# Kernel tuning notes

Hardware: AMD Instinct MI355X
Metric: run time of the kernel (lower is better)

## Reference

```python
import jax, jax.numpy as jnp
import numpy as np

D = 768
NH = 12
HD = D // NH
T = 8
HW = 14
B = 16
BT = B * T
NTOK = 1 + HW * HW  # 197
DH = int(D * 0.25)  # adapter hidden = 192
SCALE = 0.5


def _ln(x, g, b, eps=1e-5):
    # fp32 LayerNorm (matches LayerNorm subclass casting to fp32)
    xf = x.astype(jnp.float32)
    m = xf.mean(-1, keepdims=True)
    v = ((xf - m) ** 2).mean(-1, keepdims=True)
    return (((xf - m) / jnp.sqrt(v + eps)) * g + b).astype(x.dtype)


def _adapter(x, w1, b1, w2, b2, skip):
    h = jax.nn.gelu(x @ w1.T + b1, approximate=False)
    h = h @ w2.T + b2
    return x + h if skip else h


def _attention(xq, ykv, in_w, in_b, out_w, out_b):
    # xq: [Tx, N, D], ykv: [Ty, N, D]
    q = xq @ in_w[:D].T + in_b[:D]
    k = ykv @ in_w[D:2 * D].T + in_b[D:2 * D]
    v = ykv @ in_w[2 * D:].T + in_b[2 * D:]
    Tx, N, _ = q.shape
    Ty = k.shape[0]
    q = q.reshape(Tx, N, NH, HD).transpose(1, 2, 0, 3)  # [N,h,Tx,hd]
    k = k.reshape(Ty, N, NH, HD).transpose(1, 2, 0, 3)
    v = v.reshape(Ty, N, NH, HD).transpose(1, 2, 0, 3)
    aff = jnp.einsum('nhqd,nhkd->nhqk', q, k) / jnp.asarray(np.sqrt(HD), q.dtype)
    aff = jax.nn.softmax(aff, axis=-1)
    out = jnp.einsum('nhqk,nhkd->nhqd', aff, v)
    out = out.transpose(2, 0, 1, 3).reshape(Tx, N, D)
    return out @ out_w.T + out_b


_SHIFTS = (((0, 0), -4), ((0, 1), 1), ((1, 0), -1), ((0, 2), 2),
           ((2, 0), -2), ((1, 2), 3), ((2, 1), -3), ((2, 2), 4))


def _patch_shift(x):
    # x: [B, T, H, W, C]; roll along time on strided spatial grids
    out = x
    for (i, j), s in _SHIFTS:
        out = out.at[:, :, i::3, j::3, :].set(jnp.roll(x[:, :, i::3, j::3, :], s, axis=1))
    return out


def _forward(x, in_w, in_b, out_w, out_b, ln1_g, ln1_b, ln2_g, ln2_b,
             fc_w, fc_b, proj_w, proj_b,
             t1_w, t1_b, t2_w, t2_b,
             s1_w, s1_b, s2_w, s2_b,
             m1_w, m1_b, m2_w, m2_b):
    n, bt, d = x.shape
    b = bt // T
    # temporal attention on class token
    cls = x[:1]  # [1, bt, d]
    xt = cls.reshape(1, b, T, d).transpose(2, 1, 0, 3).reshape(T, b, d)
    xtn = _ln(xt, ln1_g, ln1_b)
    xt = _attention(xtn, xtn, in_w, in_b, out_w, out_b)
    xt = _adapter(xt, t1_w, t1_b, t2_w, t2_b, skip=False)
    xt = xt.reshape(T, b, 1, d).transpose(2, 1, 0, 3).reshape(1, bt, d)
    x = jnp.concatenate([x[:1], xt, x[1:]], axis=0)  # [n+1, bt, d]
    # spatial attention with patch shift (extra shifted K/V tokens)
    xln = _ln(x, ln1_g, ln1_b)
    tmp = xln[2:]  # [HW*HW, bt, d]
    tmp = tmp.reshape(HW, HW, b, T, d).transpose(2, 3, 0, 1, 4)  # b t h w c
    tmp = _patch_shift(tmp)
    tmp = tmp.transpose(2, 3, 0, 1, 4).reshape(HW * HW, bt, d)
    kv = jnp.concatenate([xln, tmp], axis=0)  # [2n+... , bt, d]
    attn_out = _attention(xln, kv, in_w, in_b, out_w, out_b)
    x = x + _adapter(attn_out, s1_w, s1_b, s2_w, s2_b, skip=True)
    # drop temporal token
    x = jnp.concatenate([x[:1], x[2:]], axis=0)
    # MLP + scaled MLP adapter
    xn = _ln(x, ln2_g, ln2_b)
    h = xn @ fc_w.T + fc_b
    h = h * jax.nn.sigmoid(1.702 * h)  # QuickGELU
    mlp = h @ proj_w.T + proj_b
    x = x + mlp + SCALE * _adapter(xn, m1_w, m1_b, m2_w, m2_b, skip=False)
    return x


def setup_inputs() -> dict:
    key = jax.random.key(0)
    ks = jax.random.split(key, 16)
    s = 0.02
    inp = {
        'x': jax.random.normal(ks[0], (NTOK, BT, D), jnp.float32),
        'in_w': jax.random.normal(ks[1], (3 * D, D), jnp.float32) * s,
        'in_b': jnp.zeros((3 * D,), jnp.float32),
        'out_w': jax.random.normal(ks[2], (D, D), jnp.float32) * s,
        'out_b': jnp.zeros((D,), jnp.float32),
        'ln1_g': jnp.ones((D,), jnp.float32),
        'ln1_b': jnp.zeros((D,), jnp.float32),
        'ln2_g': jnp.ones((D,), jnp.float32),
        'ln2_b': jnp.zeros((D,), jnp.float32),
        'fc_w': jax.random.normal(ks[3], (4 * D, D), jnp.float32) * s,
        'fc_b': jnp.zeros((4 * D,), jnp.float32),
        'proj_w': jax.random.normal(ks[4], (D, 4 * D), jnp.float32) * s,
        'proj_b': jnp.zeros((D,), jnp.float32),
        't1_w': jax.random.normal(ks[5], (DH, D), jnp.float32) * s,
        't1_b': jnp.zeros((DH,), jnp.float32),
        't2_w': jax.random.normal(ks[6], (D, DH), jnp.float32) * s,
        't2_b': jnp.zeros((D,), jnp.float32),
        's1_w': jax.random.normal(ks[7], (DH, D), jnp.float32) * s,
        's1_b': jnp.zeros((DH,), jnp.float32),
        's2_w': jax.random.normal(ks[8], (D, DH), jnp.float32) * s,
        's2_b': jnp.zeros((D,), jnp.float32),
        'm1_w': jax.random.normal(ks[9], (DH, D), jnp.float32) * s,
        'm1_b': jnp.zeros((DH,), jnp.float32),
        'm2_w': jax.random.normal(ks[10], (D, DH), jnp.float32) * s,
        'm2_b': jnp.zeros((D,), jnp.float32),
    }
    return inp


def reference(x, in_w, in_b, out_w, out_b, ln1_g, ln1_b, ln2_g, ln2_b,
              fc_w, fc_b, proj_w, proj_b,
              t1_w, t1_b, t2_w, t2_b,
              s1_w, s1_b, s2_w, s2_b,
              m1_w, m1_b, m2_w, m2_b):
    return _forward(x, in_w, in_b, out_w, out_b, ln1_g, ln1_b, ln2_g, ln2_b,
                    fc_w, fc_b, proj_w, proj_b,
                    t1_w, t1_b, t2_w, t2_b,
                    s1_w, s1_b, s2_w, s2_b,
                    m1_w, m1_b, m2_w, m2_b)
```

## Files before the change

### kernel.cpp

```cpp
#include <hip/hip_runtime.h>
#include <hip/hip_bf16.h>


#define DEV static __device__ __forceinline__

constexpr int D     = 768;
constexpr int TT    = 8;
constexpr int BT    = 128;
constexpr int NTOK  = 197;
constexpr int NTOK2 = 198;
constexpr int NKV   = 394;
constexpr int NKVP  = 448;
constexpr int NQP   = 224;
constexpr int NSZ   = 64;
constexpr int MQ    = NTOK2 * NSZ;
constexpr int MKV   = NKV   * NSZ;

constexpr int R2 = NTOK2 * BT;
constexpr int R3 = NTOK  * BT;

constexpr size_t O_WB  = 0;
constexpr size_t O_XLN = 3981312;
constexpr size_t O_AO  = O_XLN + 9732096;
constexpr size_t O_QT  = O_AO  + 9732096;
constexpr size_t O_KT  = O_QT  + 5505024;
constexpr size_t O_VT  = O_KT  + 11010048;
constexpr size_t O_SM  = O_VT  + 11010048;
constexpr size_t O_XT   = O_SM;
constexpr size_t O_XTN  = O_XT  + 98304;
constexpr size_t O_QKVT = O_XTN + 49152;
constexpr size_t O_AT   = O_QKVT+ 294912;
constexpr size_t O_ATP  = O_AT  + 49152;
constexpr size_t O_TH   = O_ATP + 49152;
constexpr size_t O_XT2  = O_TH  + 12288;
constexpr size_t O_MQ   = O_XT2 + 98304;
constexpr size_t O_MKV  = O_MQ  + 12672;

constexpr size_t WB_INW = 0;
constexpr size_t WB_OUTW= 1769472;
constexpr size_t WB_FCW = 2359296;
constexpr size_t WB_PJW = 4718592;
constexpr size_t WB_T1W = 7077888;
constexpr size_t WB_T2W = 7225344;
constexpr size_t WB_S1W = 7372800;
constexpr size_t WB_S2W = 7520256;
constexpr size_t WB_M1W = 7667712;
constexpr size_t WB_M2W = 7815168;

typedef __attribute__((ext_vector_type(8))) short bf16x8;
typedef __attribute__((ext_vector_type(4))) float f32x4;
#define MFMA16 __builtin_amdgcn_mfma_f32_16x16x32_bf16

DEV float bf2f(unsigned short u) { return __uint_as_float(((unsigned)u) << 16); }
DEV unsigned short f2bf(float f) {
    unsigned u = __float_as_uint(f);
    u += 0x7fffu + ((u >> 16) & 1u);
    return (unsigned short)(u >> 16);
}

__global__ __launch_bounds__(256) void convert_k(const float* __restrict__ src,
                                                 unsigned short* __restrict__ dst, int n)
{
    int i = blockIdx.x * 256 + threadIdx.x;
    if (i < n) dst[i] = f2bf(src[i]);
}

template<int EPI, int OMODE>
__global__ __launch_bounds__(256) void gemm_mfma_k(
    const unsigned short* __restrict__ A, const int* __restrict__ rowmap,
    const unsigned short* __restrict__ Wb, int wlda,
    const float* __restrict__ bias, float bscale,
    float* __restrict__ Yf, unsigned short* __restrict__ Yb, int N, int K)
{
    __shared__ unsigned short Als[128][40];
    __shared__ unsigned short Wls[64][40];
    const int tid = threadIdx.x;
    const int n0 = blockIdx.x * 64, m0 = blockIdx.y * 128;
    const int w = tid >> 6, l = tid & 63;

    const int sr = tid >> 2, sseg = tid & 3;
    int gr1 = m0 + sr, gr2 = m0 + 64 + sr;
    if (rowmap) { gr1 = rowmap[gr1]; gr2 = rowmap[gr2]; }
    const unsigned short* Ap1 = A + (size_t)gr1 * K + sseg * 8;
    const unsigned short* Ap2 = A + (size_t)gr2 * K + sseg * 8;
    const unsigned short* Wp  = Wb + (size_t)(n0 + sr) * wlda + sseg * 8;

    f32x4 acc[2][4];
    #pragma unroll
    for (int r = 0; r < 2; ++r)
        #pragma unroll
        for (int c = 0; c < 4; ++c)
            acc[r][c] = (f32x4){0.f, 0.f, 0.f, 0.f};

    for (int k0 = 0; k0 < K; k0 += 32) {
        __syncthreads();
        *(uint4*)&Als[sr][sseg * 8]      = *(const uint4*)(Ap1 + k0);
        *(uint4*)&Als[64 + sr][sseg * 8] = *(const uint4*)(Ap2 + k0);
        *(uint4*)&Wls[sr][sseg * 8]      = *(const uint4*)(Wp  + k0);
        __syncthreads();

        bf16x8 af[2], bfr[4];
        #pragma unroll
        for (int r = 0; r < 2; ++r)
            af[r] = *(const bf16x8*)&Als[w * 32 + r * 16 + (l & 15)][(l >> 4) * 8];
        #pragma unroll
        for (int c = 0; c < 4; ++c)
            bfr[c] = *(const bf16x8*)&Wls[c * 16 + (l & 15)][(l >> 4) * 8];
        #pragma unroll
        for (int r = 0; r < 2; ++r)
            #pragma unroll
            for (int c = 0; c < 4; ++c)
                acc[r][c] = MFMA16(af[r], bfr[c], acc[r][c], 0, 0, 0);
    }

    #pragma unroll
    for (int r = 0; r < 2; ++r) {
        #pragma unroll
        for (int c = 0; c < 4; ++c) {
            const int colg = n0 + c * 16 + (l & 15);
            const float bv = bscale * bias[colg];
            #pragma unroll
            for (int i = 0; i < 4; ++i) {
                const int rowg = m0 + w * 32 + r * 16 + ((l >> 4) << 2) + i;
                float v = acc[r][c][i] + bv;
                if (EPI == 1) v = 0.5f * v * (1.f + erff(v * 0.70710678118654752f));
                else if (EPI == 2) v = v / (1.f + __expf(-1.702f * v));
                if (OMODE == 0) {
                    Yf[(size_t)rowg * N + colg] = v;
                } else if (OMODE == 1) {
                    Yb[(size_t)rowg * N + colg] = f2bf(v);
                } else if (OMODE == 3) {
                    int j = rowg >> 6, bbl = rowg & 63, h = colg >> 6, d = colg & 63;
                    Yb[(((size_t)bbl * 12 + h) * NKVP + j) * 64 + d] = f2bf(v);
                } else if (OMODE == 4) {
                    int j = rowg >> 6, bbl = rowg & 63, h = colg >> 6, d = colg & 63;
                    Yb[(((size_t)bbl * 12 + h) * 64 + d) * NKVP + j] = f2bf(v);
                } else if (OMODE == 5) {
                    int j = rowg >> 6, bbl = rowg & 63, h = colg >> 6, d = colg & 63;
                    Yb[(((size_t)bbl * 12 + h) * NQP + j) * 64 + d] = f2bf(v * 0.125f);
                } else if (OMODE == 6) {
                    Yf[(size_t)rowg * N + colg] += v;
                } else if (OMODE == 7) {
                    Yf[(size_t)rowg * N + colg] += 0.5f * v;
                }
            }
        }
    }
}

template<typename TO>
__global__ __launch_bounds__(256) void ln_k(
    const float* __restrict__ in, TO* __restrict__ out,
    const float* __restrict__ g, const float* __restrict__ b, int rows)
{
    int w = (int)((blockIdx.x * 256 + threadIdx.x) >> 6);
    int lane = threadIdx.x & 63;
    if (w >= rows) return;
    const float* x = in + (size_t)w * D;
    float v[12];
    float s = 0.f;
    #pragma unroll
    for (int i = 0; i < 12; ++i) { v[i] = x[lane + 64 * i]; s += v[i]; }
    #pragma unroll
    for (int m = 32; m; m >>= 1) s += __shfl_xor(s, m);
    float mean = s * (1.f / 768.f);
    float s2 = 0.f;
    #pragma unroll
    for (int i = 0; i < 12; ++i) { float d0 = v[i] - mean; s2 += d0 * d0; }
    #pragma unroll
    for (int m = 32; m; m >>= 1) s2 += __shfl_xor(s2, m);
    float rstd = rsqrtf(s2 * (1.f / 768.f) + 1e-5f);
    TO* o = out + (size_t)w * D;
    #pragma unroll
    for (int i = 0; i < 12; ++i) {
        int c = lane + 64 * i;
        float y = (v[i] - mean) * rstd * g[c] + b[c];
        if constexpr (sizeof(TO) == 2) o[c] = f2bf(y); else o[c] = y;
    }
}

__global__ __launch_bounds__(256) void ln_gather_k(
    const float* __restrict__ x, const float* __restrict__ xt2,
    unsigned short* __restrict__ out,
    const float* __restrict__ g, const float* __restrict__ b)
{
    int w = (int)((blockIdx.x * 256 + threadIdx.x) >> 6);
    int lane = threadIdx.x & 63;
    if (w >= R2) return;
    int tok = w >> 7, bb = w & 127;
    const float* src;
    if (tok == 0)      src = x + (size_t)bb * D;
    else if (tok == 1) src = xt2 + (size_t)((bb & 7) * 16 + (bb >> 3)) * D;
    else               src = x + ((size_t)(tok - 1) * BT + bb) * D;
    float v[12];
    float s = 0.f;
    #pragma unroll
    for (int i = 0; i < 12; ++i) { v[i] = src[lane + 64 * i]; s += v[i]; }
    #pragma unroll
    for (int m = 32; m; m >>= 1) s += __shfl_xor(s, m);
    float mean = s * (1.f / 768.f);
    float s2 = 0.f;
    #pragma unroll
    for (int i = 0; i < 12; ++i) { float d0 = v[i] - mean; s2 += d0 * d0; }
    #pragma unroll
    for (int m = 32; m; m >>= 1) s2 += __shfl_xor(s2, m);
    float rstd = rsqrtf(s2 * (1.f / 768.f) + 1e-5f);
    unsigned short* o = out + (size_t)w * D;
    #pragma unroll
    for (int i = 0; i < 12; ++i) {
        int c = lane + 64 * i;
        o[c] = f2bf((v[i] - mean) * rstd * g[c] + b[c]);
    }
}

__global__ __launch_bounds__(256) void gather_cls_k(const float* __restrict__ x, float* __restrict__ xt)
{
    int idx = blockIdx.x * 256 + threadIdx.x;
    if (idx >= 128 * 768) return;
    int row = idx / 768, c = idx % 768;
    int t = row >> 4, bsel = row & 15;
    xt[idx] = x[(size_t)(bsel * TT + t) * D + c];
}

__global__ __launch_bounds__(64) void attn_temporal_k(
    const float* __restrict__ QKVt, unsigned short* __restrict__ Ot)
{
    int n = blockIdx.x, h = blockIdx.y;
    int lane = threadIdx.x;
    __shared__ float qs[8][64], ks[8][64], vs[8][64];
    __shared__ float ps[8][9];
    {
        int t = lane >> 3, f8 = lane & 7;
        size_t rb = ((size_t)(t * 16 + n)) * 2304 + h * 64 + f8 * 8;
        *(float4*)&qs[t][f8 * 8]     = *(const float4*)&QKVt[rb];
        *(float4*)&qs[t][f8 * 8 + 4] = *(const float4*)&QKVt[rb + 4];
        *(float4*)&ks[t][f8 * 8]     = *(const float4*)&QKVt[rb + 768];
        *(float4*)&ks[t][f8 * 8 + 4] = *(const float4*)&QKVt[rb + 772];
        *(float4*)&vs[t][f8 * 8]     = *(const float4*)&QKVt[rb + 1536];
        *(float4*)&vs[t][f8 * 8 + 4] = *(const float4*)&QKVt[rb + 1540];
    }
    __syncthreads();
    int qt = lane >> 3, kt = lane & 7;
    float s = 0.f;
    #pragma unroll
    for (int d0 = 0; d0 < 64; ++d0) s += qs[qt][d0] * ks[kt][d0];
    s *= 0.125f;
    float mx = s;
    #pragma unroll
    for (int m = 4; m; m >>= 1) mx = fmaxf(mx, __shfl_xor(mx, m));
    float p = __expf(s - mx), sum = p;
    #pragma unroll
    for (int m = 4; m; m >>= 1) sum += __shfl_xor(sum, m);
    ps[qt][kt] = p / sum;
    __syncthreads();
    int dg = lane & 7;
    float o[8] = {};
    #pragma unroll
    for (int k2 = 0; k2 < 8; ++k2) {
        float pp = ps[qt][k2];
        #pragma unroll
        for (int dd = 0; dd < 8; ++dd) o[dd] += pp * vs[k2][dg * 8 + dd];
    }
    unsigned short* op = &Ot[((size_t)(qt * 16 + n)) * D + h * 64 + dg * 8];
    #pragma unroll
    for (int dd = 0; dd < 8; ++dd) op[dd] = f2bf(o[dd]);
}

__global__ __launch_bounds__(256) void build_maps_k(int* __restrict__ mq,
                                                    int* __restrict__ mkv, int nbase)
{
    int idx = blockIdx.x * 256 + threadIdx.x;
    if (idx < MQ) {
        int j = idx >> 6, bbl = idx & 63;
        mq[idx] = j * BT + nbase + bbl;
    }
    int k = idx - MQ;
    if (k >= 0 && k < MKV) {
        int j = k >> 6, bb = nbase + (k & 63);
        int src;
        if (j < NTOK2) src = j * BT + bb;
        else {
            const int stab[9] = {-4, 1, 2, -1, 0, 3, -2, -3, 4};
            int p = j - NTOK2, r = p / 14, c = p % 14;
            int s = stab[(r % 3) * 3 + (c % 3)];
            int b = bb >> 3, t = bb & 7;
            int t2 = (t - s) & 7;
            src = (2 + p) * BT + b * TT + t2;
        }
        mkv[k] = src;
    }
}

__global__ __launch_bounds__(256) void attn_mfma_k(
    const unsigned short* __restrict__ Qt, const unsigned short* __restrict__ Kt,
    const unsigned short* __restrict__ Vt, unsigned short* __restrict__ AO, int nbase)
{
    const int qt0 = blockIdx.x * 32;
    const int h = blockIdx.y, nloc = blockIdx.z;
    const int tid = threadIdx.x, w = tid >> 6, l = tid & 63;
    __shared__ float Sls[32][68];
    __shared__ unsigned short Pls[32][72];
    __shared__ float mrun[32], lrun[32], alphals[32];

    const size_t baseQ = ((size_t)(nloc * 12 + h)) * NQP * 64;
    const size_t baseK = ((size_t)(nloc * 12 + h)) * NKVP * 64;
    const size_t baseV = ((size_t)(nloc * 12 + h)) * 64 * NKVP;

    bf16x8 qf[2][2];
    #pragma unroll
    for (int qb = 0; qb < 2; ++qb)
        #pragma unroll
        for (int ds = 0; ds < 2; ++ds)
            qf[qb][ds] = *(const bf16x8*)&Qt[baseQ + (size_t)(qt0 + qb * 16 + (l & 15)) * 64 + ds * 32 + (l >> 4) * 8];

    if (tid < 32) { mrun[tid] = -3e30f; lrun[tid] = 0.f; }
    f32x4 of[2];
    of[0] = (f32x4){0.f, 0.f, 0.f, 0.f};
    of[1] = (f32x4){0.f, 0.f, 0.f, 0.f};
    __syncthreads();

    for (int kv0 = 0; kv0 < NKV; kv0 += 64) {
        f32x4 sa[2];
        sa[0] = (f32x4){0.f, 0.f, 0.f, 0.f};
        sa[1] = (f32x4){0.f, 0.f, 0.f, 0.f};
        #pragma unroll
        for (int ds = 0; ds < 2; ++ds) {
            bf16x8 kf = *(const bf16x8*)&Kt[baseK + (size_t)(kv0 + w * 16 + (l & 15)) * 64 + ds * 32 + (l >> 4) * 8];
            #pragma unroll
            for (int qb = 0; qb < 2; ++qb)
                sa[qb] = MFMA16(qf[qb][ds], kf, sa[qb], 0, 0, 0);
        }
        #pragma unroll
        for (int qb = 0; qb < 2; ++qb)
            #pragma unroll
            for (int i = 0; i < 4; ++i)
                Sls[qb * 16 + ((l >> 4) << 2) + i][w * 16 + (l & 15)] = sa[qb][i];
        __syncthreads();

        {
            int row = tid >> 3, cg = tid & 7;
            float sv[8], pv[8];
            float mx = -3e30f;
            #pragma unroll
            for (int j = 0; j < 8; ++j) {
                int c = cg * 8 + j;
                float s = (kv0 + c < NKV) ? Sls[row][c] : -3e30f;
                sv[j] = s; mx = fmaxf(mx, s);
            }
            mx = fmaxf(mx, __shfl_xor(mx, 1));
            mx = fmaxf(mx, __shfl_xor(mx, 2));
            mx = fmaxf(mx, __shfl_xor(mx, 4));
            float mold = mrun[row];
            float mnew = fmaxf(mold, mx);
            float ps = 0.f;
            #pragma unroll
            for (int j = 0; j < 8; ++j) { float p = __expf(sv[j] - mnew); pv[j] = p; ps += p; }
            ps += __shfl_xor(ps, 1);
            ps += __shfl_xor(ps, 2);
            ps += __shfl_xor(ps, 4);
            if (cg == 0) {
                float al = __expf(mold - mnew);
                alphals[row] = al;
                mrun[row] = mnew;
                lrun[row] = lrun[row] * al + ps;
            }
            #pragma unroll
            for (int j = 0; j < 8; ++j) Pls[row][cg * 8 + j] = f2bf(pv[j]);
        }
        __syncthreads();

        #pragma unroll
        for (int qb = 0; qb < 2; ++qb) {
            #pragma unroll
            for (int i = 0; i < 4; ++i)
                of[qb][i] *= alphals[qb * 16 + ((l >> 4) << 2) + i];
        }
        #pragma unroll
        for (int ks = 0; ks < 2; ++ks) {
            bf16x8 vf = *(const bf16x8*)&Vt[baseV + (size_t)(w * 16 + (l & 15)) * NKVP + kv0 + ks * 32 + (l >> 4) * 8];
            #pragma unroll
            for (int qb = 0; qb < 2; ++qb) {
                bf16x8 pf = *(const bf16x8*)&Pls[qb * 16 + (l & 15)][ks * 32 + (l >> 4) * 8];
                of[qb] = MFMA16(pf, vf, of[qb], 0, 0, 0);
            }
        }
        __syncthreads();
    }

    #pragma unroll
    for (int qb = 0; qb < 2; ++qb) {
        #pragma unroll
        for (int i = 0; i < 4; ++i) {
            int qrow = qb * 16 + ((l >> 4) << 2) + i;
            int q = qt0 + qrow;
            if (q < NTOK2) {
                float inv = 1.f / lrun[qrow];
                AO[((size_t)q * BT + nbase + nloc) * D + h * 64 + w * 16 + (l & 15)] = f2bf(of[qb][i] * inv);
            }
        }
    }
}

__global__ __launch_bounds__(256) void residual_drop_k(
    const float* __restrict__ x, const unsigned short* __restrict__ ao2b,
    const unsigned short* __restrict__ sadb, float* __restrict__ out)
{
    int idx = blockIdx.x * 256 + threadIdx.x;
    int tok = idx / (BT * D), rest = idx % (BT * D);
    int stok = tok ? tok + 1 : 0;
    size_t s = (size_t)stok * BT * D + rest;
    size_t sx = (stok == 0) ? (size_t)rest : (size_t)(stok - 1) * BT * D + rest;
    out[idx] = x[sx] + bf2f(ao2b[s]) + bf2f(sadb[s]);
}

extern "C" void kernel_launch(void* const* d_in, const int* in_sizes, int n_in,
                              void* d_out, int out_size, void* d_ws, size_t ws_size,
                              hipStream_t stream)
{
    const float* x    = (const float*)d_in[0];
    const float* in_w = (const float*)d_in[1];
    const float* in_b = (const float*)d_in[2];
    const float* outw = (const float*)d_in[3];
    const float* outb = (const float*)d_in[4];
    const float* ln1g = (const float*)d_in[5];
    const float* ln1b = (const float*)d_in[6];
    const float* ln2g = (const float*)d_in[7];
    const float* ln2b = (const float*)d_in[8];
    const float* fcw  = (const float*)d_in[9];
    const float* fcb  = (const float*)d_in[10];
    const float* pjw  = (const float*)d_in[11];
    const float* pjb  = (const float*)d_in[12];
    const float* t1w  = (const float*)d_in[13];
    const float* t1b  = (const float*)d_in[14];
    const float* t2w  = (const float*)d_in[15];
    const float* t2b  = (const float*)d_in[16];
    const float* s1w  = (const float*)d_in[17];
    const float* s1b  = (const float*)d_in[18];
    const float* s2w  = (const float*)d_in[19];
    const float* s2b  = (const float*)d_in[20];
    const float* m1w  = (const float*)d_in[21];
    const float* m1b  = (const float*)d_in[22];
    const float* m2w  = (const float*)d_in[23];
    const float* m2b  = (const float*)d_in[24];

    float* ws  = (float*)d_ws;
    float* out = (float*)d_out;

    unsigned short* WB = (unsigned short*)(ws + O_WB);
    unsigned short* w_in  = WB + WB_INW;
    unsigned short* w_out = WB + WB_OUTW;
    unsigned short* w_fc  = WB + WB_FCW;
    unsigned short* w_pj  = WB + WB_PJW;
    unsigned short* w_t1  = WB + WB_T1W;
    unsigned short* w_t2  = WB + WB_T2W;
    unsigned short* w_s1  = WB + WB_S1W;
    unsigned short* w_s2  = WB + WB_S2W;
    unsigned short* w_m1  = WB + WB_M1W;
    unsigned short* w_m2  = WB + WB_M2W;

    unsigned short* xln  = (unsigned short*)(ws + O_XLN);
    unsigned short* AO   = (unsigned short*)(ws + O_AO);
    unsigned short* Qt   = (unsigned short*)(ws + O_QT);
    unsigned short* Kt   = (unsigned short*)(ws + O_KT);
    unsigned short* Vt   = (unsigned short*)(ws + O_VT);
    unsigned short* ao2b = xln;
    unsigned short* xn   = AO;
    unsigned short* h192 = Qt;
    unsigned short* h19m = Qt;
    unsigned short* sadb = Kt;
    unsigned short* hfcb = Vt;

    float* xt            = ws + O_XT;
    unsigned short* xtn  = (unsigned short*)(ws + O_XTN);
    float* qkvt          = ws + O_QKVT;
    unsigned short* at   = (unsigned short*)(ws + O_AT);
    unsigned short* atp  = (unsigned short*)(ws + O_ATP);
    unsigned short* th   = (unsigned short*)(ws + O_TH);
    float* xt2           = ws + O_XT2;
    int*   mapq          = (int*)(ws + O_MQ);
    int*   mapkv         = (int*)(ws + O_MKV);

    auto conv = [&](const float* s, unsigned short* dst, int n) {
        convert_k<<<(n + 255) / 256, 256, 0, stream>>>(s, dst, n);
    };
    conv(in_w, w_in, 2304 * 768);
    conv(outw, w_out, 768 * 768);
    conv(fcw,  w_fc,  3072 * 768);
    conv(pjw,  w_pj,  768 * 3072);
    conv(t1w,  w_t1,  192 * 768);
    conv(t2w,  w_t2,  768 * 192);
    conv(s1w,  w_s1,  192 * 768);
    conv(s2w,  w_s2,  768 * 192);
    conv(m1w,  w_m1,  192 * 768);
    conv(m2w,  w_m2,  768 * 192);

    gather_cls_k<<<384, 256, 0, stream>>>(x, xt);
    ln_k<unsigned short><<<32, 256, 0, stream>>>(xt, xtn, ln1g, ln1b, 128);
    gemm_mfma_k<0,0><<<dim3(36,1), 256, 0, stream>>>(xtn, nullptr, w_in, 768, in_b, 1.f, qkvt, nullptr, 2304, 768);
    attn_temporal_k<<<dim3(16,12), 64, 0, stream>>>(qkvt, at);
    gemm_mfma_k<0,1><<<dim3(12,1), 256, 0, stream>>>(at,  nullptr, w_out, 768, outb, 1.f, nullptr, atp, 768, 768);
    gemm_mfma_k<1,1><<<dim3(3,1),  256, 0, stream>>>(atp, nullptr, w_t1,  768, t1b, 1.f, nullptr, th,  192, 768);
    gemm_mfma_k<0,0><<<dim3(12,1), 256, 0, stream>>>(th,  nullptr, w_t2,  192, t2b, 1.f, xt2, nullptr, 768, 192);

    ln_gather_k<<<6336, 256, 0, stream>>>(x, xt2, xln, ln1g, ln1b);

    for (int c = 0; c < 2; ++c) {
        const int nbase = c * NSZ;
        build_maps_k<<<148, 256, 0, stream>>>(mapq, mapkv, nbase);
        gemm_mfma_k<0,5><<<dim3(12,99),  256, 0, stream>>>(xln, mapq,  w_in,              768, in_b,        1.f, nullptr, Qt, 768, 768);
        gemm_mfma_k<0,3><<<dim3(12,197), 256, 0, stream>>>(xln, mapkv, w_in + 768 * 768,  768, in_b + 768,  1.f, nullptr, Kt, 768, 768);
        gemm_mfma_k<0,4><<<dim3(12,197), 256, 0, stream>>>(xln, mapkv, w_in + 1536 * 768, 768, in_b + 1536, 1.f, nullptr, Vt, 768, 768);
        attn_mfma_k<<<dim3(7,12,64), 256, 0, stream>>>(Qt, Kt, Vt, AO, nbase);
    }

    gemm_mfma_k<0,1><<<dim3(12,198), 256, 0, stream>>>(AO,   nullptr, w_out, 768, outb, 1.f, nullptr, ao2b, 768, 768);
    gemm_mfma_k<1,1><<<dim3(3,198),  256, 0, stream>>>(ao2b, nullptr, w_s1,  768, s1b,  1.f, nullptr, h192, 192, 768);
    gemm_mfma_k<0,1><<<dim3(12,198), 256, 0, stream>>>(h192, nullptr, w_s2,  192, s2b,  1.f, nullptr, sadb, 768, 192);
    residual_drop_k<<<75648, 256, 0, stream>>>(x, ao2b, sadb, out);

    ln_k<unsigned short><<<6304, 256, 0, stream>>>(out, xn, ln2g, ln2b, R3);
    gemm_mfma_k<1,1><<<dim3(3,197),  256, 0, stream>>>(xn,   nullptr, w_m1, 768, m1b, 1.f, nullptr, h19m, 192, 768);
    gemm_mfma_k<0,7><<<dim3(12,197), 256, 0, stream>>>(h19m, nullptr, w_m2, 192, m2b, 1.f, out, nullptr, 768, 192);

    for (int q = 0; q < 4; ++q) {
        gemm_mfma_k<2,1><<<dim3(12,197), 256, 0, stream>>>(xn,   nullptr, w_fc + (size_t)q * 768 * 768, 768,  fcb + q * 768, 1.f, nullptr, hfcb, 768, 768);
        gemm_mfma_k<0,6><<<dim3(12,197), 256, 0, stream>>>(hfcb, nullptr, w_pj + q * 768,               3072, pjb, (q == 0) ? 1.f : 0.f, out, nullptr, 768, 768);
    }
}
```

Measured before the change: 1.852 ms.

## Use direct global-to-LDS loads, fuse residual epilogue, concatenate MLP and adapter GEMMs

The GEMM tile loads now use global_load_lds, which copies data straight into LDS without staging it in registers, and the LDS tile padding is removed. The residual/drop kernel is folded into the s2 GEMM epilogue. The MLP and adapter down-projections now share one concatenated K dimension with combined bias and weights, so the output accumulates in a single GEMM, chunked over M. V is stored untransposed and transposed into LDS inside attention. These changes cut kernel launches and extra passes over memory, but unpadded LDS may cause bank conflicts and the in-attention transpose adds LDS work.

Measured after the change: 1.670 ms. 9.8% less time.

```diff
diff --git a/kernel.cpp b/kernel.cpp
--- a/kernel.cpp
+++ b/kernel.cpp
@@ -15,6 +15,7 @@
 constexpr int NSZ   = 64;
 constexpr int MQ    = NTOK2 * NSZ;
 constexpr int MKV   = NKV   * NSZ;
+constexpr int KCAT  = 3264;
 
 constexpr int R2 = NTOK2 * BT;
 constexpr int R3 = NTOK  * BT;
@@ -35,17 +36,16 @@
 constexpr size_t O_XT2  = O_TH  + 12288;
 constexpr size_t O_MQ   = O_XT2 + 98304;
 constexpr size_t O_MKV  = O_MQ  + 12672;
+constexpr size_t O_CB   = O_MKV + 25216;
 
 constexpr size_t WB_INW = 0;
 constexpr size_t WB_OUTW= 1769472;
 constexpr size_t WB_FCW = 2359296;
-constexpr size_t WB_PJW = 4718592;
 constexpr size_t WB_T1W = 7077888;
 constexpr size_t WB_T2W = 7225344;
 constexpr size_t WB_S1W = 7372800;
 constexpr size_t WB_S2W = 7520256;
 constexpr size_t WB_M1W = 7667712;
-constexpr size_t WB_M2W = 7815168;
 
 typedef __attribute__((ext_vector_type(8))) short bf16x8;
 typedef __attribute__((ext_vector_type(4))) float f32x4;
@@ -58,11 +58,33 @@
     return (unsigned short)(u >> 16);
 }
 
+DEV void gll16(const unsigned short* g, unsigned short* l) {
+    __builtin_amdgcn_global_load_lds(
+        (const __attribute__((address_space(1))) void*)g,
+        (__attribute__((address_space(3))) void*)l, 16, 0, 0);
+}
+
 __global__ __launch_bounds__(256) void convert_k(const float* __restrict__ src,
                                                  unsigned short* __restrict__ dst, int n)
 {
     int i = blockIdx.x * 256 + threadIdx.x;
     if (i < n) dst[i] = f2bf(src[i]);
+}
+
+__global__ __launch_bounds__(256) void convert2d_k(const float* __restrict__ src,
+    int rows, int cols, int sld, unsigned short* __restrict__ dst, int dld, float scale)
+{
+    int i = blockIdx.x * 256 + threadIdx.x;
+    if (i >= rows * cols) return;
+    int r = i / cols, c = i % cols;
+    dst[(size_t)r * dld + c] = f2bf(src[(size_t)r * sld + c] * scale);
+}
+
+__global__ __launch_bounds__(256) void combine_bias_k(const float* __restrict__ a,
+    const float* __restrict__ b, float* __restrict__ cb)
+{
+    int i = blockIdx.x * 256 + threadIdx.x;
+    if (i < 768) cb[i] = a[i] + 0.5f * b[i];
 }
 
 template<int EPI, int OMODE>
@@ -70,20 +92,25 @@
     const unsigned short* __restrict__ A, const int* __restrict__ rowmap,
     const unsigned short* __restrict__ Wb, int wlda,
     const float* __restrict__ bias, float bscale,
-    float* __restrict__ Yf, unsigned short* __restrict__ Yb, int N, int K)
-{
-    __shared__ unsigned short Als[128][40];
-    __shared__ unsigned short Wls[64][40];
+    float* __restrict__ Yf, unsigned short* __restrict__ Yb,
+    int N, int K, int ldy, const float* __restrict__ Xf)
+{
+    __shared__ unsigned short Als[128][32];
+    __shared__ unsigned short Wls[64][32];
     const int tid = threadIdx.x;
     const int n0 = blockIdx.x * 64, m0 = blockIdx.y * 128;
     const int w = tid >> 6, l = tid & 63;
 
-    const int sr = tid >> 2, sseg = tid & 3;
-    int gr1 = m0 + sr, gr2 = m0 + 64 + sr;
-    if (rowmap) { gr1 = rowmap[gr1]; gr2 = rowmap[gr2]; }
-    const unsigned short* Ap1 = A + (size_t)gr1 * K + sseg * 8;
-    const unsigned short* Ap2 = A + (size_t)gr2 * K + sseg * 8;
-    const unsigned short* Wp  = Wb + (size_t)(n0 + sr) * wlda + sseg * 8;
+    int ga0 = m0 + w * 32 + (l >> 2);
+    int ga1 = ga0 + 16;
+    const int gw = n0 + w * 16 + (l >> 2);
+    if (rowmap) { ga0 = rowmap[ga0]; ga1 = rowmap[ga1]; }
+    const unsigned short* Ap0 = A + (size_t)ga0 * K + (l & 3) * 8;
+    const unsigned short* Ap1 = A + (size_t)ga1 * K + (l & 3) * 8;
+    const unsigned short* Wp  = Wb + (size_t)gw * wlda + (l & 3) * 8;
+    unsigned short* lA0 = &Als[w * 32 + (l >> 2)][(l & 3) * 8];
+    unsigned short* lA1 = &Als[w * 32 + 16 + (l >> 2)][(l & 3) * 8];
+    unsigned short* lW  = &Wls[w * 16 + (l >> 2)][(l & 3) * 8];
 
     f32x4 acc[2][4];
     #pragma unroll
@@ -94,9 +121,9 @@
 
     for (int k0 = 0; k0 < K; k0 += 32) {
         __syncthreads();
-        *(uint4*)&Als[sr][sseg * 8]      = *(const uint4*)(Ap1 + k0);
-        *(uint4*)&Als[64 + sr][sseg * 8] = *(const uint4*)(Ap2 + k0);
-        *(uint4*)&Wls[sr][sseg * 8]      = *(const uint4*)(Wp  + k0);
+        gll16(Ap0 + k0, lA0);
+        gll16(Ap1 + k0, lA1);
+        gll16(Wp  + k0, lW);
         __syncthreads();
 
         bf16x8 af[2], bfr[4];
@@ -126,22 +153,24 @@
                 if (EPI == 1) v = 0.5f * v * (1.f + erff(v * 0.70710678118654752f));
                 else if (EPI == 2) v = v / (1.f + __expf(-1.702f * v));
                 if (OMODE == 0) {
-                    Yf[(size_t)rowg * N + colg] = v;
+                    Yf[(size_t)rowg * ldy + colg] = v;
                 } else if (OMODE == 1) {
-                    Yb[(size_t)rowg * N + colg] = f2bf(v);
+                    Yb[(size_t)rowg * ldy + colg] = f2bf(v);
                 } else if (OMODE == 3) {
                     int j = rowg >> 6, bbl = rowg & 63, h = colg >> 6, d = colg & 63;
                     Yb[(((size_t)bbl * 12 + h) * NKVP + j) * 64 + d] = f2bf(v);
-                } else if (OMODE == 4) {
-                    int j = rowg >> 6, bbl = rowg & 63, h = colg >> 6, d = colg & 63;
-                    Yb[(((size_t)bbl * 12 + h) * 64 + d) * NKVP + j] = f2bf(v);
                 } else if (OMODE == 5) {
                     int j = rowg >> 6, bbl = rowg & 63, h = colg >> 6, d = colg & 63;
                     Yb[(((size_t)bbl * 12 + h) * NQP + j) * 64 + d] = f2bf(v * 0.125f);
                 } else if (OMODE == 6) {
-                    Yf[(size_t)rowg * N + colg] += v;
-                } else if (OMODE == 7) {
-                    Yf[(size_t)rowg * N + colg] += 0.5f * v;
+                    Yf[(size_t)rowg * ldy + colg] += v;
+                } else if (OMODE == 8) {
+                    int tok2 = rowg >> 7, bb2 = rowg & 127;
+                    if (tok2 != 1) {
+                        int otok = tok2 ? tok2 - 1 : 0;
+                        size_t oi = ((size_t)(otok * BT + bb2)) * ldy + colg;
+                        Yf[oi] = Xf[oi] + bf2f(Yb[(size_t)rowg * ldy + colg]) + v;
+                    }
                 }
             }
         }
@@ -300,11 +329,11 @@
     const int tid = threadIdx.x, w = tid >> 6, l = tid & 63;
     __shared__ float Sls[32][68];
     __shared__ unsigned short Pls[32][72];
+    __shared__ unsigned short Vls[64][72];
     __shared__ float mrun[32], lrun[32], alphals[32];
 
     const size_t baseQ = ((size_t)(nloc * 12 + h)) * NQP * 64;
     const size_t baseK = ((size_t)(nloc * 12 + h)) * NKVP * 64;
-    const size_t baseV = ((size_t)(nloc * 12 + h)) * 64 * NKVP;
 
     bf16x8 qf[2][2];
     #pragma unroll
@@ -320,6 +349,15 @@
     __syncthreads();
 
     for (int kv0 = 0; kv0 < NKV; kv0 += 64) {
+        #pragma unroll
+        for (int p = 0; p < 2; ++p) {
+            int idx = tid + p * 256;
+            int j = idx >> 3, seg = idx & 7;
+            uint4 vv = *(const uint4*)&Vt[baseK + (size_t)(kv0 + j) * 64 + seg * 8];
+            const unsigned short* pv = (const unsigned short*)&vv;
+            #pragma unroll
+            for (int e = 0; e < 8; ++e) Vls[seg * 8 + e][j] = pv[e];
+        }
         f32x4 sa[2];
         sa[0] = (f32x4){0.f, 0.f, 0.f, 0.f};
         sa[1] = (f32x4){0.f, 0.f, 0.f, 0.f};
@@ -377,7 +415,7 @@
         }
         #pragma unroll
         for (int ks = 0; ks < 2; ++ks) {
-            bf16x8 vf = *(const bf16x8*)&Vt[baseV + (size_t)(w * 16 + (l & 15)) * NKVP + kv0 + ks * 32 + (l >> 4) * 8];
+            bf16x8 vf = *(const bf16x8*)&Vls[w * 16 + (l & 15)][ks * 32 + (l >> 4) * 8];
             #pragma unroll
             for (int qb = 0; qb < 2; ++qb) {
                 bf16x8 pf = *(const bf16x8*)&Pls[qb * 16 + (l & 15)][ks * 32 + (l >> 4) * 8];
@@ -399,18 +437,6 @@
             }
         }
     }
-}
-
-__global__ __launch_bounds__(256) void residual_drop_k(
-    const float* __restrict__ x, const unsigned short* __restrict__ ao2b,
-    const unsigned short* __restrict__ sadb, float* __restrict__ out)
-{
-    int idx = blockIdx.x * 256 + threadIdx.x;
-    int tok = idx / (BT * D), rest = idx % (BT * D);
-    int stok = tok ? tok + 1 : 0;
-    size_t s = (size_t)stok * BT * D + rest;
-    size_t sx = (stok == 0) ? (size_t)rest : (size_t)(stok - 1) * BT * D + rest;
-    out[idx] = x[sx] + bf2f(ao2b[s]) + bf2f(sadb[s]);
 }
 
 extern "C" void kernel_launch(void* const* d_in, const int* in_sizes, int n_in,
@@ -450,13 +476,11 @@
     unsigned short* w_in  = WB + WB_INW;
     unsigned short* w_out = WB + WB_OUTW;
     unsigned short* w_fc  = WB + WB_FCW;
-    unsigned short* w_pj  = WB + WB_PJW;
     unsigned short* w_t1  = WB + WB_T1W;
     unsigned short* w_t2  = WB + WB_T2W;
     unsigned short* w_s1  = WB + WB_S1W;
     unsigned short* w_s2  = WB + WB_S2W;
     unsigned short* w_m1  = WB + WB_M1W;
-    unsigned short* w_m2  = WB + WB_M2W;
 
     unsigned short* xln  = (unsigned short*)(ws + O_XLN);
     unsigned short* AO   = (unsigned short*)(ws + O_AO);
@@ -466,9 +490,8 @@
     unsigned short* ao2b = xln;
     unsigned short* xn   = AO;
     unsigned short* h192 = Qt;
-    unsigned short* h19m = Qt;
-    unsigned short* sadb = Kt;
-    unsigned short* hfcb = Vt;
+    unsigned short* pjcat= (unsigned short*)(ws + O_QT + 2433024);
+    unsigned short* catb = Kt;
 
     float* xt            = ws + O_XT;
     unsigned short* xtn  = (unsigned short*)(ws + O_XTN);
@@ -479,6 +502,7 @@
     float* xt2           = ws + O_XT2;
     int*   mapq          = (int*)(ws + O_MQ);
     int*   mapkv         = (int*)(ws + O_MKV);
+    float* cb            = ws + O_CB;
 
     auto conv = [&](const float* s, unsigned short* dst, int n) {
         convert_k<<<(n + 255) / 256, 256, 0, stream>>>(s, dst, n);
@@ -486,44 +510,47 @@
     conv(in_w, w_in, 2304 * 768);
     conv(outw, w_out, 768 * 768);
     conv(fcw,  w_fc,  3072 * 768);
-    conv(pjw,  w_pj,  768 * 3072);
     conv(t1w,  w_t1,  192 * 768);
     conv(t2w,  w_t2,  768 * 192);
     conv(s1w,  w_s1,  192 * 768);
     conv(s2w,  w_s2,  768 * 192);
     conv(m1w,  w_m1,  192 * 768);
-    conv(m2w,  w_m2,  768 * 192);
+    combine_bias_k<<<3, 256, 0, stream>>>(pjb, m2b, cb);
 
     gather_cls_k<<<384, 256, 0, stream>>>(x, xt);
     ln_k<unsigned short><<<32, 256, 0, stream>>>(xt, xtn, ln1g, ln1b, 128);
-    gemm_mfma_k<0,0><<<dim3(36,1), 256, 0, stream>>>(xtn, nullptr, w_in, 768, in_b, 1.f, qkvt, nullptr, 2304, 768);
+    gemm_mfma_k<0,0><<<dim3(36,1), 256, 0, stream>>>(xtn, nullptr, w_in, 768, in_b, 1.f, qkvt, nullptr, 2304, 768, 2304, nullptr);
     attn_temporal_k<<<dim3(16,12), 64, 0, stream>>>(qkvt, at);
-    gemm_mfma_k<0,1><<<dim3(12,1), 256, 0, stream>>>(at,  nullptr, w_out, 768, outb, 1.f, nullptr, atp, 768, 768);
-    gemm_mfma_k<1,1><<<dim3(3,1),  256, 0, stream>>>(atp, nullptr, w_t1,  768, t1b, 1.f, nullptr, th,  192, 768);
-    gemm_mfma_k<0,0><<<dim3(12,1), 256, 0, stream>>>(th,  nullptr, w_t2,  192, t2b, 1.f, xt2, nullptr, 768, 192);
+    gemm_mfma_k<0,1><<<dim3(12,1), 256, 0, stream>>>(at,  nullptr, w_out, 768, outb, 1.f, nullptr, atp, 768, 768, 768, nullptr);
+    gemm_mfma_k<1,1><<<dim3(3,1),  256, 0, stream>>>(atp, nullptr, w_t1,  768, t1b, 1.f, nullptr, th,  192, 768, 192, nullptr);
+    gemm_mfma_k<0,0><<<dim3(12,1), 256, 0, stream>>>(th,  nullptr, w_t2,  192, t2b, 1.f, xt2, nullptr, 768, 192, 768, nullptr);
 
     ln_gather_k<<<6336, 256, 0, stream>>>(x, xt2, xln, ln1g, ln1b);
 
     for (int c = 0; c < 2; ++c) {
         const int nbase = c * NSZ;
         build_maps_k<<<148, 256, 0, stream>>>(mapq, mapkv, nbase);
-        gemm_mfma_k<0,5><<<dim3(12,99),  256, 0, stream>>>(xln, mapq,  w_in,              768, in_b,        1.f, nullptr, Qt, 768, 768);
-        gemm_mfma_k<0,3><<<dim3(12,197), 256, 0, stream>>>(xln, mapkv, w_in + 768 * 768,  768, in_b + 768,  1.f, nullptr, Kt, 768, 768);
-        gemm_mfma_k<0,4><<<dim3(12,197), 256, 0, stream>>>(xln, mapkv, w_in + 1536 * 768, 768, in_b + 1536, 1.f, nullptr, Vt, 768, 768);
+        gemm_mfma_k<0,5><<<dim3(12,99),  256, 0, stream>>>(xln, mapq,  w_in,              768, in_b,        1.f, nullptr, Qt, 768, 768, 768, nullptr);
+        gemm_mfma_k<0,3><<<dim3(12,197), 256, 0, stream>>>(xln, mapkv, w_in + 768 * 768,  768, in_b + 768,  1.f, nullptr, Kt, 768, 768, 768, nullptr);
+        gemm_mfma_k<0,3><<<dim3(12,197), 256, 0, stream>>>(xln, mapkv, w_in + 1536 * 768, 768, in_b + 1536, 1.f, nullptr, Vt, 768, 768, 768, nullptr);
         attn_mfma_k<<<dim3(7,12,64), 256, 0, stream>>>(Qt, Kt, Vt, AO, nbase);
     }
 
-    gemm_mfma_k<0,1><<<dim3(12,198), 256, 0, stream>>>(AO,   nullptr, w_out, 768, outb, 1.f, nullptr, ao2b, 768, 768);
-    gemm_mfma_k<1,1><<<dim3(3,198),  256, 0, stream>>>(ao2b, nullptr, w_s1,  768, s1b,  1.f, nullptr, h192, 192, 768);
-    gemm_mfma_k<0,1><<<dim3(12,198), 256, 0, stream>>>(h192, nullptr, w_s2,  192, s2b,  1.f, nullptr, sadb, 768, 192);
-    residual_drop_k<<<75648, 256, 0, stream>>>(x, ao2b, sadb, out);
+    convert2d_k<<<9216, 256, 0, stream>>>(pjw, 768, 3072, 3072, pjcat, KCAT, 1.f);
+    convert2d_k<<<576,  256, 0, stream>>>(m2w, 768, 192, 192, pjcat + 3072, KCAT, 0.5f);
+
+    gemm_mfma_k<0,1><<<dim3(12,198), 256, 0, stream>>>(AO,   nullptr, w_out, 768, outb, 1.f, nullptr, ao2b, 768, 768, 768, nullptr);
+    gemm_mfma_k<1,1><<<dim3(3,198),  256, 0, stream>>>(ao2b, nullptr, w_s1,  768, s1b,  1.f, nullptr, h192, 192, 768, 192, nullptr);
+    gemm_mfma_k<0,8><<<dim3(12,198), 256, 0, stream>>>(h192, nullptr, w_s2,  192, s2b,  1.f, out, ao2b, 768, 192, 768, x);
 
     ln_k<unsigned short><<<6304, 256, 0, stream>>>(out, xn, ln2g, ln2b, R3);
-    gemm_mfma_k<1,1><<<dim3(3,197),  256, 0, stream>>>(xn,   nullptr, w_m1, 768, m1b, 1.f, nullptr, h19m, 192, 768);
-    gemm_mfma_k<0,7><<<dim3(12,197), 256, 0, stream>>>(h19m, nullptr, w_m2, 192, m2b, 1.f, out, nullptr, 768, 192);
-
-    for (int q = 0; q < 4; ++q) {
-        gemm_mfma_k<2,1><<<dim3(12,197), 256, 0, stream>>>(xn,   nullptr, w_fc + (size_t)q * 768 * 768, 768,  fcb + q * 768, 1.f, nullptr, hfcb, 768, 768);
-        gemm_mfma_k<0,6><<<dim3(12,197), 256, 0, stream>>>(hfcb, nullptr, w_pj + q * 768,               3072, pjb, (q == 0) ? 1.f : 0.f, out, nullptr, 768, 768);
-    }
-}
+    const int nbm[4] = {49, 49, 49, 50};
+    int moff = 0;
+    for (int mc = 0; mc < 4; ++mc) {
+        const int nb = nbm[mc];
+        gemm_mfma_k<2,1><<<dim3(48,nb), 256, 0, stream>>>(xn + (size_t)moff * 768, nullptr, w_fc, 768, fcb, 1.f, nullptr, catb, 3072, 768, KCAT, nullptr);
+        gemm_mfma_k<1,1><<<dim3(3,nb),  256, 0, stream>>>(xn + (size_t)moff * 768, nullptr, w_m1, 768, m1b, 1.f, nullptr, catb + 3072, 192, 768, KCAT, nullptr);
+        gemm_mfma_k<0,6><<<dim3(12,nb), 256, 0, stream>>>(catb, nullptr, pjcat, KCAT, cb, 1.f, out + (size_t)moff * 768, nullptr, 768, KCAT, 768, nullptr);
+        moff += nb * 128;
+    }
+}
```
